# Performance work log

Hardware: AMD Instinct MI355X
Metric: run time of the kernel (lower is better)

Reference implementation:

```python
import jax, jax.numpy as jnp
import numpy as np

N = 50000
E = 800000
IN_DIM = 128
HID = 128
OUT_DIM = 64


def _xavier(key, fan_in, fan_out):
    # matches nn.init.xavier_uniform_ on a (out, in) weight
    limit = float(np.sqrt(6.0 / (fan_in + fan_out)))
    return jax.random.uniform(key, (fan_in, fan_out), jnp.float32, -limit, limit)


def setup_inputs() -> dict:
    key = jax.random.key(0)
    ks = jax.random.split(key, 7)
    X = jax.random.normal(ks[0], (N, IN_DIM), jnp.float32)
    edge_row = jax.random.randint(ks[1], (E,), 0, N, jnp.int32)
    edge_col = jax.random.randint(ks[2], (E,), 0, N, jnp.int32)
    edge_weight = jax.random.uniform(ks[3], (E,), jnp.float32)
    W1 = _xavier(ks[4], IN_DIM, HID)
    b1 = jnp.zeros((HID,), jnp.float32)
    W2 = _xavier(ks[5], HID, HID)
    b2 = jnp.zeros((HID,), jnp.float32)
    W3 = _xavier(ks[6], HID, OUT_DIM)
    b3 = jnp.zeros((OUT_DIM,), jnp.float32)
    return {"X": X, "edge_row": edge_row, "edge_col": edge_col,
            "edge_weight": edge_weight,
            "W1": W1, "b1": b1, "W2": W2, "b2": b2, "W3": W3, "b3": b3}


def _spmm(edge_row, edge_col, edge_weight, H):
    # sparse A @ H via gather + segment_sum (COO SpMM)
    msgs = edge_weight[:, None] * H[edge_col]  # [E, d]
    return jax.ops.segment_sum(msgs, edge_row, num_segments=N)


def reference(X, edge_row, edge_col, edge_weight, W1, b1, W2, b2, W3, b3):
    # layer 1: SpMM -> linear -> relu (dropout disabled: eval mode)
    h = _spmm(edge_row, edge_col, edge_weight, X)
    h = jax.nn.relu(h @ W1 + b1)
    # layer 2
    h = _spmm(edge_row, edge_col, edge_weight, h)
    h = jax.nn.relu(h @ W2 + b2)
    # layer 3 (no activation)
    h = _spmm(edge_row, edge_col, edge_weight, h)
    return h @ W3 + b3
```

## Files before the change

### kernel.cpp

```cpp
#include <hip/hip_runtime.h>


typedef unsigned int uint32;
using bf16x8 = __attribute__((ext_vector_type(8))) short;
using f32x4  = __attribute__((ext_vector_type(4))) float;

static constexpr int BCAP = 3072;

static __device__ __forceinline__ unsigned short f2bf(float x) {
    unsigned int u = __builtin_bit_cast(unsigned int, x);
    u += 0x7FFFu + ((u >> 16) & 1u);
    return (unsigned short)(u >> 16);
}
static __device__ __forceinline__ float bflo(uint32 u) {
    return __builtin_bit_cast(float, u << 16);
}
static __device__ __forceinline__ float bfhi(uint32 u) {
    return __builtin_bit_cast(float, u & 0xFFFF0000u);
}

__global__ __launch_bounds__(256) void prep_kernel(const float* __restrict__ W1,
                                                   const float* __restrict__ W2,
                                                   const float* __restrict__ W3,
                                                   unsigned short* __restrict__ Wt1,
                                                   unsigned short* __restrict__ Wt2,
                                                   unsigned short* __restrict__ Wt3,
                                                   int* __restrict__ bcur, int nb) {
    int gid = blockIdx.x * 256 + threadIdx.x;
    if (gid < nb) bcur[gid] = 0;
    if (gid < 16384) {
        Wt1[gid] = f2bf(W1[(gid & 127) * 128 + (gid >> 7)]);
    } else if (gid < 32768) {
        int g = gid - 16384;
        Wt2[g] = f2bf(W2[(g & 127) * 128 + (g >> 7)]);
    } else if (gid < 40960) {
        int g = gid - 32768;
        Wt3[g] = f2bf(W3[(g & 127) * 64 + (g >> 7)]);
    }
}

__global__ __launch_bounds__(256) void bucket_scatter_kernel(const int* __restrict__ erow,
                                                             const int* __restrict__ ecol,
                                                             const float* __restrict__ ew,
                                                             int* __restrict__ bcur,
                                                             int2* __restrict__ ebuf, int e) {
    __shared__ int hist[512];
    __shared__ int psc[256];
    __shared__ int fixup[512];
    __shared__ int2 stage[4096];
    int t = threadIdx.x;
    hist[t] = 0; hist[t + 256] = 0;
    __syncthreads();
    int base = blockIdx.x * 4096;
    int4 rows[4];
#pragma unroll
    for (int j = 0; j < 4; j++) {
        int idx = base + j * 1024 + t * 4;
        int4 r = make_int4(-1, -1, -1, -1);
        if (idx + 3 < e) {
            r = *reinterpret_cast<const int4*>(&erow[idx]);
        } else {
            if (idx < e)     r.x = erow[idx];
            if (idx + 1 < e) r.y = erow[idx + 1];
            if (idx + 2 < e) r.z = erow[idx + 2];
            if (idx + 3 < e) r.w = erow[idx + 3];
        }
        rows[j] = r;
        if (r.x >= 0) atomicAdd(&hist[r.x >> 7], 1);
        if (r.y >= 0) atomicAdd(&hist[r.y >> 7], 1);
        if (r.z >= 0) atomicAdd(&hist[r.z >> 7], 1);
        if (r.w >= 0) atomicAdd(&hist[r.w >> 7], 1);
    }
    __syncthreads();
    int c0 = hist[2 * t], c1 = hist[2 * t + 1];
    int s = c0 + c1;
    psc[t] = s;
    __syncthreads();
    for (int off = 1; off < 256; off <<= 1) {
        int u = (t >= off) ? psc[t - off] : 0;
        __syncthreads();
        psc[t] += u;
        __syncthreads();
    }
    int lo0 = psc[t] - s;
    int lo1 = lo0 + c0;
    if (c0) fixup[2 * t]     = 2 * t * BCAP       + atomicAdd(&bcur[2 * t], c0)     - lo0;
    if (c1) fixup[2 * t + 1] = (2 * t + 1) * BCAP + atomicAdd(&bcur[2 * t + 1], c1) - lo1;
    __syncthreads();
    hist[2 * t] = lo0; hist[2 * t + 1] = lo1;
    __syncthreads();
#pragma unroll
    for (int j = 0; j < 4; j++) {
        int idx = base + j * 1024 + t * 4;
        int4 r = rows[j];
        int4 c = make_int4(0, 0, 0, 0);
        float4 w = make_float4(0.f, 0.f, 0.f, 0.f);
        if (idx + 3 < e) {
            c = *reinterpret_cast<const int4*>(&ecol[idx]);
            w = *reinterpret_cast<const float4*>(&ew[idx]);
        } else {
            if (idx < e)     { c.x = ecol[idx];     w.x = ew[idx]; }
            if (idx + 1 < e) { c.y = ecol[idx + 1]; w.y = ew[idx + 1]; }
            if (idx + 2 < e) { c.z = ecol[idx + 2]; w.z = ew[idx + 2]; }
            if (idx + 3 < e) { c.w = ecol[idx + 3]; w.w = ew[idx + 3]; }
        }
        if (r.x >= 0) { int b = r.x >> 7; int sl = atomicAdd(&hist[b], 1);
            stage[sl] = make_int2((b << 23) | ((r.x & 127) << 16) | c.x, __builtin_bit_cast(int, w.x)); }
        if (r.y >= 0) { int b = r.y >> 7; int sl = atomicAdd(&hist[b], 1);
            stage[sl] = make_int2((b << 23) | ((r.y & 127) << 16) | c.y, __builtin_bit_cast(int, w.y)); }
        if (r.z >= 0) { int b = r.z >> 7; int sl = atomicAdd(&hist[b], 1);
            stage[sl] = make_int2((b << 23) | ((r.z & 127) << 16) | c.z, __builtin_bit_cast(int, w.z)); }
        if (r.w >= 0) { int b = r.w >> 7; int sl = atomicAdd(&hist[b], 1);
            stage[sl] = make_int2((b << 23) | ((r.w & 127) << 16) | c.w, __builtin_bit_cast(int, w.w)); }
    }
    __syncthreads();
    int ecnt = min(4096, e - base);
    for (int i = t; i < ecnt; i += 256) {
        int2 v = stage[i];
        int b = ((unsigned)v.x) >> 23;
        int gpos = fixup[b] + i;
        if (gpos - b * BCAP < BCAP) ebuf[gpos] = v;
    }
}

__global__ __launch_bounds__(256) void bucket_sort_kernel(const int* __restrict__ bcur,
                                                          const int2* __restrict__ ebuf,
                                                          int2* __restrict__ ecsr,
                                                          int* __restrict__ row_ptr,
                                                          int n, int nb) {
    __shared__ int sc[512];
    __shared__ int2 stage[BCAP];
    __shared__ int2 sorted[BCAP];
    __shared__ int rc[128], rs[128], c2[128];
    int b = blockIdx.x;
    int t = threadIdx.x;
    sc[t]       = (t < nb)       ? min(bcur[t], BCAP)       : 0;
    sc[t + 256] = (t + 256 < nb) ? min(bcur[t + 256], BCAP) : 0;
    if (t < 128) { rc[t] = 0; c2[t] = 0; }
    __syncthreads();
    for (int off = 1; off < 512; off <<= 1) {
        int a0 = (t >= off) ? sc[t - off] : 0;
        int a1 = (t + 256 >= off) ? sc[t + 256 - off] : 0;
        __syncthreads();
        sc[t] += a0; sc[t + 256] += a1;
        __syncthreads();
    }
    int off_b = (b == 0) ? 0 : sc[b - 1];
    int cnt = sc[b] - off_b;
    if (b == 0 && t == 0) row_ptr[n] = sc[nb - 1];
    for (int i = t; i < cnt; i += 256) {
        int2 v = ebuf[b * BCAP + i];
        stage[i] = v;
        atomicAdd(&rc[(v.x >> 16) & 127], 1);
    }
    __syncthreads();
    if (t < 128) rs[t] = rc[t];
    __syncthreads();
    for (int o = 1; o < 128; o <<= 1) {
        int u = 0;
        if (t < 128 && t >= o) u = rs[t - o];
        __syncthreads();
        if (t < 128) rs[t] += u;
        __syncthreads();
    }
    if (t < 128) {
        int gr = b * 128 + t;
        if (gr < n) row_ptr[gr] = off_b + rs[t] - rc[t];
    }
    __syncthreads();
    for (int i = t; i < cnt; i += 256) {
        int2 v = stage[i];
        int r = (v.x >> 16) & 127;
        int pos = rs[r] - rc[r] + atomicAdd(&c2[r], 1);
        sorted[pos] = make_int2(v.x & 0xFFFF, v.y);
    }
    __syncthreads();
    for (int i = t; i < cnt; i += 256) ecsr[off_b + i] = sorted[i];
}

template <bool AF32, int NOUT>
__global__ __launch_bounds__(256) void gemm_mfma_kernel(const void* __restrict__ Ap,
                                                        const unsigned short* __restrict__ Wt,
                                                        unsigned short* __restrict__ Zb, int n) {
    constexpr int CT = NOUT / 16;
    int wave = threadIdx.x >> 6;
    int lane = threadIdx.x & 63;
    int m0 = blockIdx.x * 64 + wave * 16;
    int r = lane & 15;
    int g = lane >> 4;
    int arow = min(m0 + r, n - 1);
    f32x4 acc[CT] = {};
#pragma unroll
    for (int kt = 0; kt < 4; kt++) {
        int k0 = kt * 32 + g * 8;
        bf16x8 a;
        if constexpr (AF32) {
            const float* A = (const float*)Ap;
            float4 x0 = *reinterpret_cast<const float4*>(&A[(size_t)arow * 128 + k0]);
            float4 x1 = *reinterpret_cast<const float4*>(&A[(size_t)arow * 128 + k0 + 4]);
            a[0] = (short)f2bf(x0.x); a[1] = (short)f2bf(x0.y);
            a[2] = (short)f2bf(x0.z); a[3] = (short)f2bf(x0.w);
            a[4] = (short)f2bf(x1.x); a[5] = (short)f2bf(x1.y);
            a[6] = (short)f2bf(x1.z); a[7] = (short)f2bf(x1.w);
        } else {
            const unsigned short* A = (const unsigned short*)Ap;
            a = *reinterpret_cast<const bf16x8*>(&A[(size_t)arow * 128 + k0]);
        }
#pragma unroll
        for (int c = 0; c < CT; c++) {
            bf16x8 bb = *reinterpret_cast<const bf16x8*>(&Wt[(size_t)(c * 16 + r) * 128 + k0]);
            acc[c] = __builtin_amdgcn_mfma_f32_16x16x32_bf16(a, bb, acc[c], 0, 0, 0);
        }
    }
#pragma unroll
    for (int c = 0; c < CT; c++) {
#pragma unroll
        for (int rr = 0; rr < 4; rr++) {
            int row = m0 + g * 4 + rr;
            if (row < n) Zb[(size_t)row * NOUT + c * 16 + r] = f2bf(acc[c][rr]);
        }
    }
}

__global__ __launch_bounds__(256) void spmm128_kernel(const int* __restrict__ row_ptr,
                                                      const int2* __restrict__ ecw,
                                                      const unsigned short* __restrict__ Zb,
                                                      const float* __restrict__ bias,
                                                      unsigned short* __restrict__ Hb, int n) {
    int row = (blockIdx.x * 256 + threadIdx.x) >> 6;
    int lane = threadIdx.x & 63;
    if (row >= n) return;
    int beg = __builtin_amdgcn_readfirstlane(row_ptr[row]);
    int end = __builtin_amdgcn_readfirstlane(row_ptr[row + 1]);
    int deg = end - beg;
    const unsigned short* zb = Zb + (lane << 1);
    float a0 = 0.f, a1 = 0.f;
    int i = 0;
    for (; i + 4 <= deg; i += 4) {
        int2 e0 = ecw[beg + i];
        int2 e1 = ecw[beg + i + 1];
        int2 e2 = ecw[beg + i + 2];
        int2 e3 = ecw[beg + i + 3];
        uint32 z0 = *reinterpret_cast<const uint32*>(zb + ((size_t)(uint32)e0.x << 7));
        uint32 z1 = *reinterpret_cast<const uint32*>(zb + ((size_t)(uint32)e1.x << 7));
        uint32 z2 = *reinterpret_cast<const uint32*>(zb + ((size_t)(uint32)e2.x << 7));
        uint32 z3 = *reinterpret_cast<const uint32*>(zb + ((size_t)(uint32)e3.x << 7));
        float w0 = __builtin_bit_cast(float, e0.y);
        float w1 = __builtin_bit_cast(float, e1.y);
        float w2 = __builtin_bit_cast(float, e2.y);
        float w3 = __builtin_bit_cast(float, e3.y);
        a0 = fmaf(w0, bflo(z0), a0); a1 = fmaf(w0, bfhi(z0), a1);
        a0 = fmaf(w1, bflo(z1), a0); a1 = fmaf(w1, bfhi(z1), a1);
        a0 = fmaf(w2, bflo(z2), a0); a1 = fmaf(w2, bfhi(z2), a1);
        a0 = fmaf(w3, bflo(z3), a0); a1 = fmaf(w3, bfhi(z3), a1);
    }
    for (; i < deg; i++) {
        int2 e = ecw[beg + i];
        uint32 z = *reinterpret_cast<const uint32*>(zb + ((size_t)(uint32)e.x << 7));
        float w = __builtin_bit_cast(float, e.y);
        a0 = fmaf(w, bflo(z), a0); a1 = fmaf(w, bfhi(z), a1);
    }
    float2 bv = *reinterpret_cast<const float2*>(&bias[lane << 1]);
    a0 = fmaxf(a0 + bv.x, 0.f);
    a1 = fmaxf(a1 + bv.y, 0.f);
    uint32 pk = (uint32)f2bf(a0) | ((uint32)f2bf(a1) << 16);
    *reinterpret_cast<uint32*>(&Hb[(size_t)row * 128 + (lane << 1)]) = pk;
}

__global__ __launch_bounds__(256) void spmm64_kernel(const int* __restrict__ row_ptr,
                                                     const int2* __restrict__ ecw,
                                                     const unsigned short* __restrict__ Zb,
                                                     const float* __restrict__ bias,
                                                     float* __restrict__ out, int n, int e) {
    int gw = (blockIdx.x * 256 + threadIdx.x) >> 6;
    int lane = threadIdx.x & 63;
    int half = lane >> 5;
    int hl = lane & 31;
    int row = gw * 2 + half;
    bool rv = (row < n);
    int beg = 0, end = 0;
    if (rv) { beg = row_ptr[row]; end = row_ptr[row + 1]; }
    int beg0 = __builtin_amdgcn_readlane(beg, 0);
    int deg0 = __builtin_amdgcn_readlane(end, 0) - beg0;
    int beg1 = __builtin_amdgcn_readlane(beg, 32);
    int deg1 = __builtin_amdgcn_readlane(end, 32) - beg1;
    int mdeg = max(deg0, deg1);
    const unsigned short* zb = Zb + (hl << 1);
    float a0 = 0.f, a1 = 0.f;
    for (int i = 0; i < mdeg; i++) {
        int iA = min(beg0 + min(i, max(deg0 - 1, 0)), e - 1);
        int iB = min(beg1 + min(i, max(deg1 - 1, 0)), e - 1);
        int2 eA = ecw[iA];
        int2 eB = ecw[iB];
        float wA = (i < deg0) ? __builtin_bit_cast(float, eA.y) : 0.f;
        float wB = (i < deg1) ? __builtin_bit_cast(float, eB.y) : 0.f;
        int col = half ? eB.x : eA.x;
        float w = half ? wB : wA;
        uint32 z = *reinterpret_cast<const uint32*>(zb + ((size_t)(uint32)col << 6));
        a0 = fmaf(w, bflo(z), a0);
        a1 = fmaf(w, bfhi(z), a1);
    }
    if (rv) {
        float2 bv = *reinterpret_cast<const float2*>(&bias[hl << 1]);
        float2 v = make_float2(a0 + bv.x, a1 + bv.y);
        *reinterpret_cast<float2*>(&out[(size_t)row * 64 + (hl << 1)]) = v;
    }
}

extern "C" void kernel_launch(void* const* d_in, const int* in_sizes, int n_in,
                              void* d_out, int out_size, void* d_ws, size_t ws_size,
                              hipStream_t stream) {
    const float* X    = (const float*)d_in[0];
    const int*   erow = (const int*)d_in[1];
    const int*   ecol = (const int*)d_in[2];
    const float* ew   = (const float*)d_in[3];
    const float* W1   = (const float*)d_in[4];
    const float* b1   = (const float*)d_in[5];
    const float* W2   = (const float*)d_in[6];
    const float* b2   = (const float*)d_in[7];
    const float* W3   = (const float*)d_in[8];
    const float* b3   = (const float*)d_in[9];
    float* out = (float*)d_out;

    const int n = in_sizes[0] / 128;
    const int e = in_sizes[1];
    const int nb = (n + 127) >> 7;

    char* p = (char*)d_ws;
    auto alloc = [&](size_t bytes) {
        void* r = (void*)p;
        p += (bytes + 255) & ~(size_t)255;
        return r;
    };
    int*            row_ptr = (int*)alloc((size_t)(n + 1) * sizeof(int));
    int*            bcur    = (int*)alloc((size_t)nb * sizeof(int));
    int2*           ebuf    = (int2*)alloc((size_t)nb * BCAP * sizeof(int2));
    int2*           ecsr    = (int2*)alloc((size_t)e * sizeof(int2));
    unsigned short* Zb      = (unsigned short*)alloc((size_t)n * 128 * sizeof(unsigned short));
    unsigned short* Hb      = (unsigned short*)alloc((size_t)n * 128 * sizeof(unsigned short));
    unsigned short* Wt1     = (unsigned short*)alloc(128 * 128 * sizeof(unsigned short));
    unsigned short* Wt2     = (unsigned short*)alloc(128 * 128 * sizeof(unsigned short));
    unsigned short* Wt3     = (unsigned short*)alloc(64 * 128 * sizeof(unsigned short));

    const int eb4k = (e + 4095) / 4096;
    const int gemm_grid = (n + 63) / 64;
    const int sp128_grid = (n + 3) / 4;
    const int sp64_grid  = ((n + 1) / 2 + 3) / 4;

    prep_kernel<<<160, 256, 0, stream>>>(W1, W2, W3, Wt1, Wt2, Wt3, bcur, nb);
    bucket_scatter_kernel<<<eb4k, 256, 0, stream>>>(erow, ecol, ew, bcur, ebuf, e);
    bucket_sort_kernel<<<nb, 256, 0, stream>>>(bcur, ebuf, ecsr, row_ptr, n, nb);

    gemm_mfma_kernel<true, 128><<<gemm_grid, 256, 0, stream>>>(X, Wt1, Zb, n);
    spmm128_kernel<<<sp128_grid, 256, 0, stream>>>(row_ptr, ecsr, Zb, b1, Hb, n);

    gemm_mfma_kernel<false, 128><<<gemm_grid, 256, 0, stream>>>(Hb, Wt2, Zb, n);
    spmm128_kernel<<<sp128_grid, 256, 0, stream>>>(row_ptr, ecsr, Zb, b2, Hb, n);

    gemm_mfma_kernel<false, 64><<<gemm_grid, 256, 0, stream>>>(Hb, Wt3, Zb, n);
    spmm64_kernel<<<sp64_grid, 256, 0, stream>>>(row_ptr, ecsr, Zb, b3, out, n, e);
}
```

Before: 196.0 us.

## Pack CSR edges to 32-bit and split SpMM rows across column slices with shuffles

Edge entries are packed into one 32-bit word: a 16-bit column index plus a bf16 weight. This halves CSR storage and the edge-stream traffic. Both SpMM kernels now assign each row to one wave per 64-byte feature slice. The wave loads up to 64 edges in one coalesced read and broadcasts them with shuffles, so four lane groups each gather a different edge's 64-byte segment, then the groups are reduced with xor-shuffles. This trades more blocks and redundant edge reads per slice for better gather parallelism, and it adds bf16 rounding on the edge weights and a 16-bit column limit (N=50000 fits).

```diff
diff --git a/kernel.cpp b/kernel.cpp
--- a/kernel.cpp
+++ b/kernel.cpp
@@ -105,13 +105,13 @@
             if (idx + 3 < e) { c.w = ecol[idx + 3]; w.w = ew[idx + 3]; }
         }
         if (r.x >= 0) { int b = r.x >> 7; int sl = atomicAdd(&hist[b], 1);
-            stage[sl] = make_int2((b << 23) | ((r.x & 127) << 16) | c.x, __builtin_bit_cast(int, w.x)); }
+            stage[sl] = make_int2((b << 23) | ((r.x & 127) << 16) | c.x, (int)f2bf(w.x)); }
         if (r.y >= 0) { int b = r.y >> 7; int sl = atomicAdd(&hist[b], 1);
-            stage[sl] = make_int2((b << 23) | ((r.y & 127) << 16) | c.y, __builtin_bit_cast(int, w.y)); }
+            stage[sl] = make_int2((b << 23) | ((r.y & 127) << 16) | c.y, (int)f2bf(w.y)); }
         if (r.z >= 0) { int b = r.z >> 7; int sl = atomicAdd(&hist[b], 1);
-            stage[sl] = make_int2((b << 23) | ((r.z & 127) << 16) | c.z, __builtin_bit_cast(int, w.z)); }
+            stage[sl] = make_int2((b << 23) | ((r.z & 127) << 16) | c.z, (int)f2bf(w.z)); }
         if (r.w >= 0) { int b = r.w >> 7; int sl = atomicAdd(&hist[b], 1);
-            stage[sl] = make_int2((b << 23) | ((r.w & 127) << 16) | c.w, __builtin_bit_cast(int, w.w)); }
+            stage[sl] = make_int2((b << 23) | ((r.w & 127) << 16) | c.w, (int)f2bf(w.w)); }
     }
     __syncthreads();
     int ecnt = min(4096, e - base);
@@ -125,12 +125,12 @@
 
 __global__ __launch_bounds__(256) void bucket_sort_kernel(const int* __restrict__ bcur,
                                                           const int2* __restrict__ ebuf,
-                                                          int2* __restrict__ ecsr,
+                                                          int* __restrict__ ecsr,
                                                           int* __restrict__ row_ptr,
                                                           int n, int nb) {
     __shared__ int sc[512];
     __shared__ int2 stage[BCAP];
-    __shared__ int2 sorted[BCAP];
+    __shared__ int sorted[BCAP];
     __shared__ int rc[128], rs[128], c2[128];
     int b = blockIdx.x;
     int t = threadIdx.x;
@@ -172,7 +172,7 @@
         int2 v = stage[i];
         int r = (v.x >> 16) & 127;
         int pos = rs[r] - rc[r] + atomicAdd(&c2[r], 1);
-        sorted[pos] = make_int2(v.x & 0xFFFF, v.y);
+        sorted[pos] = (v.y << 16) | (v.x & 0xFFFF);
     }
     __syncthreads();
     for (int i = t; i < cnt; i += 256) ecsr[off_b + i] = sorted[i];
@@ -223,87 +223,94 @@
 }
 
 __global__ __launch_bounds__(256) void spmm128_kernel(const int* __restrict__ row_ptr,
-                                                      const int2* __restrict__ ecw,
+                                                      const int* __restrict__ ecw,
                                                       const unsigned short* __restrict__ Zb,
                                                       const float* __restrict__ bias,
                                                       unsigned short* __restrict__ Hb, int n) {
-    int row = (blockIdx.x * 256 + threadIdx.x) >> 6;
+    int slice = blockIdx.x & 3;
+    int row = (((blockIdx.x >> 2) * 256) + threadIdx.x) >> 6;
     int lane = threadIdx.x & 63;
     if (row >= n) return;
-    int beg = __builtin_amdgcn_readfirstlane(row_ptr[row]);
-    int end = __builtin_amdgcn_readfirstlane(row_ptr[row + 1]);
-    int deg = end - beg;
-    const unsigned short* zb = Zb + (lane << 1);
+    int beg = row_ptr[row], end = row_ptr[row + 1];
+    const int grp = lane >> 4;
+    const int gl  = lane & 15;
+    const char* zbase = (const char*)Zb + (slice << 6) + (gl << 2);
     float a0 = 0.f, a1 = 0.f;
-    int i = 0;
-    for (; i + 4 <= deg; i += 4) {
-        int2 e0 = ecw[beg + i];
-        int2 e1 = ecw[beg + i + 1];
-        int2 e2 = ecw[beg + i + 2];
-        int2 e3 = ecw[beg + i + 3];
-        uint32 z0 = *reinterpret_cast<const uint32*>(zb + ((size_t)(uint32)e0.x << 7));
-        uint32 z1 = *reinterpret_cast<const uint32*>(zb + ((size_t)(uint32)e1.x << 7));
-        uint32 z2 = *reinterpret_cast<const uint32*>(zb + ((size_t)(uint32)e2.x << 7));
-        uint32 z3 = *reinterpret_cast<const uint32*>(zb + ((size_t)(uint32)e3.x << 7));
-        float w0 = __builtin_bit_cast(float, e0.y);
-        float w1 = __builtin_bit_cast(float, e1.y);
-        float w2 = __builtin_bit_cast(float, e2.y);
-        float w3 = __builtin_bit_cast(float, e3.y);
-        a0 = fmaf(w0, bflo(z0), a0); a1 = fmaf(w0, bfhi(z0), a1);
-        a0 = fmaf(w1, bflo(z1), a0); a1 = fmaf(w1, bfhi(z1), a1);
-        a0 = fmaf(w2, bflo(z2), a0); a1 = fmaf(w2, bfhi(z2), a1);
-        a0 = fmaf(w3, bflo(z3), a0); a1 = fmaf(w3, bfhi(z3), a1);
-    }
-    for (; i < deg; i++) {
-        int2 e = ecw[beg + i];
-        uint32 z = *reinterpret_cast<const uint32*>(zb + ((size_t)(uint32)e.x << 7));
-        float w = __builtin_bit_cast(float, e.y);
-        a0 = fmaf(w, bflo(z), a0); a1 = fmaf(w, bfhi(z), a1);
-    }
-    float2 bv = *reinterpret_cast<const float2*>(&bias[lane << 1]);
-    a0 = fmaxf(a0 + bv.x, 0.f);
-    a1 = fmaxf(a1 + bv.y, 0.f);
-    uint32 pk = (uint32)f2bf(a0) | ((uint32)f2bf(a1) << 16);
-    *reinterpret_cast<uint32*>(&Hb[(size_t)row * 128 + (lane << 1)]) = pk;
+    for (int wb = beg; wb < end; wb += 64) {
+        int rem = min(end - wb, 64);
+        int mv = (lane < rem) ? ecw[wb + lane] : 0;
+        int nc = (rem + 3) >> 2;
+        for (int c0 = 0; c0 < nc; c0 += 4) {
+            int v0 = __shfl(mv, (c0 + 0) * 4 + grp, 64);
+            int v1 = __shfl(mv, (c0 + 1) * 4 + grp, 64);
+            int v2 = __shfl(mv, (c0 + 2) * 4 + grp, 64);
+            int v3 = __shfl(mv, (c0 + 3) * 4 + grp, 64);
+            uint32 z0 = *reinterpret_cast<const uint32*>(zbase + ((size_t)(uint32)(v0 & 0xFFFF) << 8));
+            uint32 z1 = *reinterpret_cast<const uint32*>(zbase + ((size_t)(uint32)(v1 & 0xFFFF) << 8));
+            uint32 z2 = *reinterpret_cast<const uint32*>(zbase + ((size_t)(uint32)(v2 & 0xFFFF) << 8));
+            uint32 z3 = *reinterpret_cast<const uint32*>(zbase + ((size_t)(uint32)(v3 & 0xFFFF) << 8));
+            float w0 = bfhi((uint32)v0), w1 = bfhi((uint32)v1);
+            float w2 = bfhi((uint32)v2), w3 = bfhi((uint32)v3);
+            a0 = fmaf(w0, bflo(z0), a0); a1 = fmaf(w0, bfhi(z0), a1);
+            a0 = fmaf(w1, bflo(z1), a0); a1 = fmaf(w1, bfhi(z1), a1);
+            a0 = fmaf(w2, bflo(z2), a0); a1 = fmaf(w2, bfhi(z2), a1);
+            a0 = fmaf(w3, bflo(z3), a0); a1 = fmaf(w3, bfhi(z3), a1);
+        }
+    }
+    a0 += __shfl_xor(a0, 16, 64); a0 += __shfl_xor(a0, 32, 64);
+    a1 += __shfl_xor(a1, 16, 64); a1 += __shfl_xor(a1, 32, 64);
+    if (lane < 16) {
+        int d = (slice << 5) + (gl << 1);
+        float2 bv = *reinterpret_cast<const float2*>(&bias[d]);
+        a0 = fmaxf(a0 + bv.x, 0.f);
+        a1 = fmaxf(a1 + bv.y, 0.f);
+        uint32 pk = (uint32)f2bf(a0) | ((uint32)f2bf(a1) << 16);
+        *reinterpret_cast<uint32*>(&Hb[(size_t)row * 128 + d]) = pk;
+    }
 }
 
 __global__ __launch_bounds__(256) void spmm64_kernel(const int* __restrict__ row_ptr,
-                                                     const int2* __restrict__ ecw,
+                                                     const int* __restrict__ ecw,
                                                      const unsigned short* __restrict__ Zb,
                                                      const float* __restrict__ bias,
-                                                     float* __restrict__ out, int n, int e) {
-    int gw = (blockIdx.x * 256 + threadIdx.x) >> 6;
+                                                     float* __restrict__ out, int n) {
+    int slice = blockIdx.x & 1;
+    int row = (((blockIdx.x >> 1) * 256) + threadIdx.x) >> 6;
     int lane = threadIdx.x & 63;
-    int half = lane >> 5;
-    int hl = lane & 31;
-    int row = gw * 2 + half;
-    bool rv = (row < n);
-    int beg = 0, end = 0;
-    if (rv) { beg = row_ptr[row]; end = row_ptr[row + 1]; }
-    int beg0 = __builtin_amdgcn_readlane(beg, 0);
-    int deg0 = __builtin_amdgcn_readlane(end, 0) - beg0;
-    int beg1 = __builtin_amdgcn_readlane(beg, 32);
-    int deg1 = __builtin_amdgcn_readlane(end, 32) - beg1;
-    int mdeg = max(deg0, deg1);
-    const unsigned short* zb = Zb + (hl << 1);
+    if (row >= n) return;
+    int beg = row_ptr[row], end = row_ptr[row + 1];
+    const int grp = lane >> 4;
+    const int gl  = lane & 15;
+    const char* zbase = (const char*)Zb + (slice << 6) + (gl << 2);
     float a0 = 0.f, a1 = 0.f;
-    for (int i = 0; i < mdeg; i++) {
-        int iA = min(beg0 + min(i, max(deg0 - 1, 0)), e - 1);
-        int iB = min(beg1 + min(i, max(deg1 - 1, 0)), e - 1);
-        int2 eA = ecw[iA];
-        int2 eB = ecw[iB];
-        float wA = (i < deg0) ? __builtin_bit_cast(float, eA.y) : 0.f;
-        float wB = (i < deg1) ? __builtin_bit_cast(float, eB.y) : 0.f;
-        int col = half ? eB.x : eA.x;
-        float w = half ? wB : wA;
-        uint32 z = *reinterpret_cast<const uint32*>(zb + ((size_t)(uint32)col << 6));
-        a0 = fmaf(w, bflo(z), a0);
-        a1 = fmaf(w, bfhi(z), a1);
-    }
-    if (rv) {
-        float2 bv = *reinterpret_cast<const float2*>(&bias[hl << 1]);
+    for (int wb = beg; wb < end; wb += 64) {
+        int rem = min(end - wb, 64);
+        int mv = (lane < rem) ? ecw[wb + lane] : 0;
+        int nc = (rem + 3) >> 2;
+        for (int c0 = 0; c0 < nc; c0 += 4) {
+            int v0 = __shfl(mv, (c0 + 0) * 4 + grp, 64);
+            int v1 = __shfl(mv, (c0 + 1) * 4 + grp, 64);
+            int v2 = __shfl(mv, (c0 + 2) * 4 + grp, 64);
+            int v3 = __shfl(mv, (c0 + 3) * 4 + grp, 64);
+            uint32 z0 = *reinterpret_cast<const uint32*>(zbase + ((size_t)(uint32)(v0 & 0xFFFF) << 7));
+            uint32 z1 = *reinterpret_cast<const uint32*>(zbase + ((size_t)(uint32)(v1 & 0xFFFF) << 7));
+            uint32 z2 = *reinterpret_cast<const uint32*>(zbase + ((size_t)(uint32)(v2 & 0xFFFF) << 7));
+            uint32 z3 = *reinterpret_cast<const uint32*>(zbase + ((size_t)(uint32)(v3 & 0xFFFF) << 7));
+            float w0 = bfhi((uint32)v0), w1 = bfhi((uint32)v1);
+            float w2 = bfhi((uint32)v2), w3 = bfhi((uint32)v3);
+            a0 = fmaf(w0, bflo(z0), a0); a1 = fmaf(w0, bfhi(z0), a1);
+            a0 = fmaf(w1, bflo(z1), a0); a1 = fmaf(w1, bfhi(z1), a1);
+            a0 = fmaf(w2, bflo(z2), a0); a1 = fmaf(w2, bfhi(z2), a1);
+            a0 = fmaf(w3, bflo(z3), a0); a1 = fmaf(w3, bfhi(z3), a1);
+        }
+    }
+    a0 += __shfl_xor(a0, 16, 64); a0 += __shfl_xor(a0, 32, 64);
+    a1 += __shfl_xor(a1, 16, 64); a1 += __shfl_xor(a1, 32, 64);
+    if (lane < 16) {
+        int d = (slice << 5) + (gl << 1);
+        float2 bv = *reinterpret_cast<const float2*>(&bias[d]);
         float2 v = make_float2(a0 + bv.x, a1 + bv.y);
-        *reinterpret_cast<float2*>(&out[(size_t)row * 64 + (hl << 1)]) = v;
+        *reinterpret_cast<float2*>(&out[(size_t)row * 64 + d]) = v;
     }
 }
 
@@ -335,7 +342,7 @@
     int*            row_ptr = (int*)alloc((size_t)(n + 1) * sizeof(int));
     int*            bcur    = (int*)alloc((size_t)nb * sizeof(int));
     int2*           ebuf    = (int2*)alloc((size_t)nb * BCAP * sizeof(int2));
-    int2*           ecsr    = (int2*)alloc((size_t)e * sizeof(int2));
+    int*            ecsr    = (int*)alloc((size_t)e * sizeof(int));
     unsigned short* Zb      = (unsigned short*)alloc((size_t)n * 128 * sizeof(unsigned short));
     unsigned short* Hb      = (unsigned short*)alloc((size_t)n * 128 * sizeof(unsigned short));
     unsigned short* Wt1     = (unsigned short*)alloc(128 * 128 * sizeof(unsigned short));
@@ -343,9 +350,10 @@
     unsigned short* Wt3     = (unsigned short*)alloc(64 * 128 * sizeof(unsigned short));
 
     const int eb4k = (e + 4095) / 4096;
-    const int gemm_grid = (n + 63) / 64;
-    const int sp128_grid = (n + 3) / 4;
-    const int sp64_grid  = ((n + 1) / 2 + 3) / 4;
+    const int gemm_grid  = (n + 63) / 64;
+    const int rb         = (n + 3) / 4;
+    const int sp128_grid = rb * 4;
+    const int sp64_grid  = rb * 2;
 
     prep_kernel<<<160, 256, 0, stream>>>(W1, W2, W3, Wt1, Wt2, Wt3, bcur, nb);
     bucket_scatter_kernel<<<eb4k, 256, 0, stream>>>(erow, ecol, ew, bcur, ebuf, e);
@@ -358,5 +366,5 @@
     spmm128_kernel<<<sp128_grid, 256, 0, stream>>>(row_ptr, ecsr, Zb, b2, Hb, n);
 
     gemm_mfma_kernel<false, 64><<<gemm_grid, 256, 0, stream>>>(Hb, Wt3, Zb, n);
-    spmm64_kernel<<<sp64_grid, 256, 0, stream>>>(row_ptr, ecsr, Zb, b3, out, n, e);
-}
+    spmm64_kernel<<<sp64_grid, 256, 0, stream>>>(row_ptr, ecsr, Zb, b3, out, n);
+}
```

Result: slower. 246.3 us (+25.6%).
